# Optimization experiments

Hardware: AMD Instinct MI355X
Metric: run time of the kernel (lower is better)

The kernel has to match this reference:

```python
import jax, jax.numpy as jnp
import numpy as np

N_NODES = 50000
N_EDGES = 800000
D_IN = 512
D_OUT = 256


def setup_inputs() -> dict:
    key = jax.random.key(0)
    k1, k2, k3, k4, k5 = jax.random.split(key, 5)
    x = jax.random.normal(k1, (N_NODES, D_IN), dtype=jnp.float32)
    W = jax.random.normal(k2, (D_IN, D_OUT), dtype=jnp.float32) * (1.0 / np.sqrt(D_IN))
    edge_vals = jax.random.uniform(k3, (N_EDGES,), dtype=jnp.float32)
    edge_src = jax.random.randint(k4, (N_EDGES,), 0, N_NODES, dtype=jnp.int64)
    edge_dst = jax.random.randint(k5, (N_EDGES,), 0, N_NODES, dtype=jnp.int64)
    return {"x": x, "W": W, "edge_vals": edge_vals,
            "edge_src": edge_src, "edge_dst": edge_dst}


def reference(x, W, edge_vals, edge_src, edge_dst):
    # Dense feature transform: h = X W   [N, D_OUT]
    h = jnp.matmul(x, W)
    # Sparse adjacency matmul (A @ h) in COO form:
    # out[d] = sum_{e: dst[e]==d} vals[e] * h[src[e]]
    msgs = h[edge_src] * edge_vals[:, None]  # [E, D_OUT]
    agg = jax.ops.segment_sum(msgs, edge_dst, num_segments=N_NODES)
    # Activation ('relu')
    return jax.nn.relu(agg)
```

## Files before the change

kernel.cpp:

```cpp
#include <hip/hip_runtime.h>

typedef unsigned short u16;
typedef unsigned int   u32;
typedef __attribute__((ext_vector_type(8))) short bf16x8;
typedef __attribute__((ext_vector_type(4))) float f32x4;
typedef __attribute__((ext_vector_type(4))) unsigned short u16x4;

#define N_NODES 50000
#define N_EDGES 800000
#define D_IN    512
#define D_OUT   256
#define M_PAD   50048
#define NB_SCAN 196

__device__ __forceinline__ u16 f2bf(float f) {
  u32 u = __float_as_uint(f);
  return (u16)((u + 0x7FFFu + ((u >> 16) & 1u)) >> 16);
}
__device__ __forceinline__ u32 f2bf2(float lo, float hi) {
  return (u32)f2bf(lo) | ((u32)f2bf(hi) << 16);
}
__device__ __forceinline__ float bf2f(u16 h) {
  return __uint_as_float(((u32)h) << 16);
}

__device__ __forceinline__ void gload_lds16(const void* g, void* l) {
  __builtin_amdgcn_global_load_lds(
      (const __attribute__((address_space(1))) unsigned int*)g,
      (__attribute__((address_space(3))) unsigned int*)l, 16, 0, 0);
}

__global__ void k_init(int* __restrict__ counts, const float* __restrict__ W,
                       u16* __restrict__ wt) {
  int b = blockIdx.x;
  if (b < NB_SCAN) {
    int i = b * 256 + threadIdx.x;
    if (i < N_NODES) counts[i] = 0;
  } else {
    int g = (b - NB_SCAN) * 256 + threadIdx.x;
    int n = g & 255, k = g >> 8;
    wt[n * D_IN + k] = f2bf(W[k * D_OUT + n]);
  }
}

__global__ __launch_bounds__(512) void k_gemm_hist(
    const float* __restrict__ X, const u16* __restrict__ Bt,
    u16* __restrict__ C, int M,
    const int* __restrict__ edst, int* __restrict__ counts,
    int* __restrict__ rank, int E, int ngemm) {
  if ((int)blockIdx.x >= ngemm) {
    int e = ((int)blockIdx.x - ngemm) * 512 + threadIdx.x;
    if (e < E) rank[e] = atomicAdd(&counts[edst[e]], 1);
    return;
  }

  __shared__ u16 As[128 * 64];
  __shared__ u16 Bs[256 * 64];
  int tid  = threadIdx.x;
  int wave = tid >> 6, lane = tid & 63;
  int m0 = blockIdx.x * 128;
  int wr = wave >> 2, wc = wave & 3;
  int r = lane & 15, q = lane >> 4;

  int arow = tid >> 2, aq = tid & 3;
  int grow = m0 + arow;
  bool avalid = grow < M;
  const float* xrow = X + (size_t)grow * D_IN + aq * 16;
  u16* adst = As + arow * 64 + aq * 16;

  f32x4 acc[4][4];
#pragma unroll
  for (int i = 0; i < 4; ++i)
#pragma unroll
    for (int j = 0; j < 4; ++j) acc[i][j] = (f32x4){0.f, 0.f, 0.f, 0.f};

  for (int k0 = 0; k0 < D_IN; k0 += 64) {
#pragma unroll
    for (int j = 0; j < 4; ++j) {
      int c = tid + j * 512;
      int brow = c >> 3, bk = c & 7;
      gload_lds16(Bt + (size_t)brow * D_IN + k0 + bk * 8, Bs + c * 8);
    }
    uint4 w0 = {0u,0u,0u,0u}, w1 = {0u,0u,0u,0u};
    if (avalid) {
      float4 f0 = *(const float4*)(xrow + k0);
      float4 f1 = *(const float4*)(xrow + k0 + 4);
      float4 f2 = *(const float4*)(xrow + k0 + 8);
      float4 f3 = *(const float4*)(xrow + k0 + 12);
      w0.x = f2bf2(f0.x, f0.y);  w0.y = f2bf2(f0.z, f0.w);
      w0.z = f2bf2(f1.x, f1.y);  w0.w = f2bf2(f1.z, f1.w);
      w1.x = f2bf2(f2.x, f2.y);  w1.y = f2bf2(f2.z, f2.w);
      w1.z = f2bf2(f3.x, f3.y);  w1.w = f2bf2(f3.z, f3.w);
    }
    *(uint4*)(adst)     = w0;
    *(uint4*)(adst + 8) = w1;
    __syncthreads();
#pragma unroll
    for (int kk = 0; kk < 2; ++kk) {
      bf16x8 a[4], b[4];
#pragma unroll
      for (int i = 0; i < 4; ++i)
        a[i] = *(const bf16x8*)(As + (wr * 64 + i * 16 + r) * 64 + kk * 32 + q * 8);
#pragma unroll
      for (int j = 0; j < 4; ++j)
        b[j] = *(const bf16x8*)(Bs + (wc * 64 + j * 16 + r) * 64 + kk * 32 + q * 8);
#pragma unroll
      for (int i = 0; i < 4; ++i)
#pragma unroll
        for (int j = 0; j < 4; ++j)
          acc[i][j] = __builtin_amdgcn_mfma_f32_16x16x32_bf16(a[i], b[j], acc[i][j], 0, 0, 0);
    }
    __syncthreads();
  }

#pragma unroll
  for (int i = 0; i < 4; ++i)
#pragma unroll
    for (int j = 0; j < 4; ++j)
#pragma unroll
      for (int t2 = 0; t2 < 4; ++t2) {
        int row = m0 + wr * 64 + i * 16 + q * 4 + t2;
        int col = wc * 64 + j * 16 + r;
        if (row < M) C[(size_t)row * D_OUT + col] = f2bf(acc[i][j][t2]);
      }
}

__global__ void k_scan1(const int* __restrict__ counts, int* __restrict__ row_start,
                        int* __restrict__ btot, int n) {
  __shared__ int buf[256];
  int t = threadIdx.x;
  int i = blockIdx.x * 256 + t;
  int c = (i < n) ? counts[i] : 0;
  buf[t] = c;
  __syncthreads();
#pragma unroll
  for (int off = 1; off < 256; off <<= 1) {
    int v = (t >= off) ? buf[t - off] : 0;
    __syncthreads();
    buf[t] += v;
    __syncthreads();
  }
  if (i < n) row_start[i + 1] = buf[t];
  if (t == 255) btot[blockIdx.x] = buf[255];
}

__global__ void k_scan2(int* __restrict__ btot, int nb) {
  __shared__ int buf[256];
  int t = threadIdx.x;
  int c = (t < nb) ? btot[t] : 0;
  buf[t] = c;
  __syncthreads();
#pragma unroll
  for (int off = 1; off < 256; off <<= 1) {
    int v = (t >= off) ? buf[t - off] : 0;
    __syncthreads();
    buf[t] += v;
    __syncthreads();
  }
  if (t < nb) btot[t] = buf[t] - c;
}

__global__ void k_scan3(int* __restrict__ row_start, const int* __restrict__ btot, int n) {
  int i = blockIdx.x * blockDim.x + threadIdx.x;
  if (i < n) row_start[i + 1] += btot[i >> 8];
  if (i == 0) row_start[0] = 0;
}

__global__ void k_scatter(const int* __restrict__ esrc, const int* __restrict__ edst,
                          const float* __restrict__ ev, const int* __restrict__ row_start,
                          const int* __restrict__ rank,
                          int2* __restrict__ pack, int E) {
  int e = blockIdx.x * blockDim.x + threadIdx.x;
  if (e < E) {
    int pos = row_start[edst[e]] + rank[e];
    pack[pos] = make_int2(esrc[e], __float_as_int(ev[e]));
  }
}

__global__ __launch_bounds__(256) void k_agg(
    const u16* __restrict__ hb, const int* __restrict__ row_start,
    const int2* __restrict__ pack, float* __restrict__ out, int n_nodes) {
  int wave = threadIdx.x >> 6, lane = threadIdx.x & 63;
  int node = blockIdx.x * 4 + wave;
  if (node >= n_nodes) return;
  int s0 = row_start[node], s1 = row_start[node + 1];
  int cnt = s1 - s0;

  f32x4 a0 = {0.f,0.f,0.f,0.f}, a1 = {0.f,0.f,0.f,0.f};
  f32x4 a2 = {0.f,0.f,0.f,0.f}, a3 = {0.f,0.f,0.f,0.f};
  size_t lane8 = (size_t)lane * 8;

  for (int base = 0; base < cnt; base += 64) {
    int m = cnt - base; if (m > 64) m = 64;
    int   msrc = 0;
    float mval = 0.f;
    if (lane < m) {
      int2 p = pack[s0 + base + lane];
      msrc = p.x;
      mval = __uint_as_float((u32)p.y);
    }
    int k = 0;
    for (; k + 16 <= m; k += 16) {
      int   s[16];
      float v[16];
#pragma unroll
      for (int j = 0; j < 16; ++j) {
        s[j] = __shfl(msrc, k + j);
        v[j] = __shfl(mval, k + j);
      }
      u16x4 h[16];
#pragma unroll
      for (int j = 0; j < 16; ++j)
        h[j] = *(const u16x4*)((const char*)hb + (((size_t)(u32)s[j]) << 9) + lane8);
#pragma unroll
      for (int j = 0; j < 16; ++j) {
        f32x4* a = (j & 2) ? ((j & 1) ? &a3 : &a2) : ((j & 1) ? &a1 : &a0);
        (*a)[0] += v[j] * bf2f(h[j][0]);
        (*a)[1] += v[j] * bf2f(h[j][1]);
        (*a)[2] += v[j] * bf2f(h[j][2]);
        (*a)[3] += v[j] * bf2f(h[j][3]);
      }
    }
    for (; k + 4 <= m; k += 4) {
      int   s[4];
      float v[4];
#pragma unroll
      for (int j = 0; j < 4; ++j) {
        s[j] = __shfl(msrc, k + j);
        v[j] = __shfl(mval, k + j);
      }
      u16x4 h[4];
#pragma unroll
      for (int j = 0; j < 4; ++j)
        h[j] = *(const u16x4*)((const char*)hb + (((size_t)(u32)s[j]) << 9) + lane8);
#pragma unroll
      for (int j = 0; j < 4; ++j) {
        f32x4* a = (j & 1) ? &a1 : &a0;
        (*a)[0] += v[j] * bf2f(h[j][0]);
        (*a)[1] += v[j] * bf2f(h[j][1]);
        (*a)[2] += v[j] * bf2f(h[j][2]);
        (*a)[3] += v[j] * bf2f(h[j][3]);
      }
    }
    for (; k < m; ++k) {
      int   s = __shfl(msrc, k);
      float v = __shfl(mval, k);
      u16x4 h = *(const u16x4*)((const char*)hb + (((size_t)(u32)s) << 9) + lane8);
      a0[0] += v * bf2f(h[0]);
      a0[1] += v * bf2f(h[1]);
      a0[2] += v * bf2f(h[2]);
      a0[3] += v * bf2f(h[3]);
    }
  }
  float4 o;
  o.x = fmaxf(a0[0] + a1[0] + a2[0] + a3[0], 0.f);
  o.y = fmaxf(a0[1] + a1[1] + a2[1] + a3[1], 0.f);
  o.z = fmaxf(a0[2] + a1[2] + a2[2] + a3[2], 0.f);
  o.w = fmaxf(a0[3] + a1[3] + a2[3] + a3[3], 0.f);
  *(float4*)(out + (size_t)node * D_OUT + lane * 4) = o;
}

extern "C" void kernel_launch(void* const* d_in, const int* in_sizes, int n_in,
                              void* d_out, int out_size, void* d_ws, size_t ws_size,
                              hipStream_t stream) {
  const float* x    = (const float*)d_in[0];
  const float* W    = (const float*)d_in[1];
  const float* ev   = (const float*)d_in[2];
  const int*   esrc = (const int*)d_in[3];
  const int*   edst = (const int*)d_in[4];
  float* out = (float*)d_out;

  char* ws = (char*)d_ws;
  size_t off = 0;
  auto alloc = [&](size_t bytes) -> void* {
    off = (off + 255) & ~(size_t)255;
    void* p = ws + off;
    off += bytes;
    return p;
  };
  u16*   wt        = (u16*)  alloc((size_t)D_OUT * D_IN * 2);
  u16*   hb        = (u16*)  alloc((size_t)N_NODES * D_OUT * 2);
  int*   counts    = (int*)  alloc((size_t)N_NODES * 4);
  int*   row_start = (int*)  alloc((size_t)(N_NODES + 1) * 4);
  int*   rank      = (int*)  alloc((size_t)N_EDGES * 4);
  int*   btot      = (int*)  alloc(256 * 4);
  int2*  pack      = (int2*) alloc((size_t)N_EDGES * 8);

  int ngemm = M_PAD / 128;
  int nhist = (N_EDGES + 511) / 512;

  k_init<<<NB_SCAN + (D_IN * D_OUT) / 256, 256, 0, stream>>>(counts, W, wt);
  k_gemm_hist<<<ngemm + nhist, 512, 0, stream>>>(x, wt, hb, N_NODES,
                                                 edst, counts, rank, N_EDGES, ngemm);
  k_scan1<<<NB_SCAN, 256, 0, stream>>>(counts, row_start, btot, N_NODES);
  k_scan2<<<1, 256, 0, stream>>>(btot, NB_SCAN);
  k_scan3<<<NB_SCAN, 256, 0, stream>>>(row_start, btot, N_NODES);
  k_scatter<<<N_EDGES / 256, 256, 0, stream>>>(esrc, edst, ev, row_start, rank, pack, N_EDGES);
  k_agg<<<(N_NODES + 3) / 4, 256, 0, stream>>>(hb, row_start, pack, out, N_NODES);
}
```

Measured before the change: 139.0 us.

## Swizzle GEMM LDS tiles and gather two edges per wave with 16-byte loads

The GEMM stores and reads its A and B LDS tiles with an XOR swizzle on the 8-element k-chunk index. This is meant to remove LDS bank conflicts on the MFMA operand reads. The aggregation kernel now splits each wave into two half-waves, each handling a different edge and loading 16 bytes (8 bf16) per lane instead of 8, then combines the halves with a cross-half shuffle. This halves the number of gather instructions per edge and issues wider loads, at the cost of fewer independent accumulators and an extra reduction step.

```diff
diff --git a/kernel.cpp b/kernel.cpp
--- a/kernel.cpp
+++ b/kernel.cpp
@@ -4,7 +4,7 @@
 typedef unsigned int   u32;
 typedef __attribute__((ext_vector_type(8))) short bf16x8;
 typedef __attribute__((ext_vector_type(4))) float f32x4;
-typedef __attribute__((ext_vector_type(4))) unsigned short u16x4;
+typedef __attribute__((ext_vector_type(8))) unsigned short u16x8;
 
 #define N_NODES 50000
 #define N_EDGES 800000
@@ -66,7 +66,8 @@
   int grow = m0 + arow;
   bool avalid = grow < M;
   const float* xrow = X + (size_t)grow * D_IN + aq * 16;
-  u16* adst = As + arow * 64 + aq * 16;
+  u16* adst0 = As + arow * 64 + (((aq * 2)     ^ (arow & 7)) * 8);
+  u16* adst1 = As + arow * 64 + (((aq * 2 + 1) ^ (arow & 7)) * 8);
 
   f32x4 acc[4][4];
 #pragma unroll
@@ -78,7 +79,8 @@
 #pragma unroll
     for (int j = 0; j < 4; ++j) {
       int c = tid + j * 512;
-      int brow = c >> 3, bk = c & 7;
+      int brow = c >> 3, bslot = c & 7;
+      int bk = bslot ^ (brow & 7);
       gload_lds16(Bt + (size_t)brow * D_IN + k0 + bk * 8, Bs + c * 8);
     }
     uint4 w0 = {0u,0u,0u,0u}, w1 = {0u,0u,0u,0u};
@@ -92,18 +94,22 @@
       w1.x = f2bf2(f2.x, f2.y);  w1.y = f2bf2(f2.z, f2.w);
       w1.z = f2bf2(f3.x, f3.y);  w1.w = f2bf2(f3.z, f3.w);
     }
-    *(uint4*)(adst)     = w0;
-    *(uint4*)(adst + 8) = w1;
+    *(uint4*)(adst0) = w0;
+    *(uint4*)(adst1) = w1;
     __syncthreads();
 #pragma unroll
     for (int kk = 0; kk < 2; ++kk) {
       bf16x8 a[4], b[4];
 #pragma unroll
-      for (int i = 0; i < 4; ++i)
-        a[i] = *(const bf16x8*)(As + (wr * 64 + i * 16 + r) * 64 + kk * 32 + q * 8);
-#pragma unroll
-      for (int j = 0; j < 4; ++j)
-        b[j] = *(const bf16x8*)(Bs + (wc * 64 + j * 16 + r) * 64 + kk * 32 + q * 8);
+      for (int i = 0; i < 4; ++i) {
+        int ar = wr * 64 + i * 16 + r;
+        a[i] = *(const bf16x8*)(As + ar * 64 + (((kk * 4 + q) ^ (ar & 7)) * 8));
+      }
+#pragma unroll
+      for (int j = 0; j < 4; ++j) {
+        int br = wc * 64 + j * 16 + r;
+        b[j] = *(const bf16x8*)(Bs + br * 64 + (((kk * 4 + q) ^ (br & 7)) * 8));
+      }
 #pragma unroll
       for (int i = 0; i < 4; ++i)
 #pragma unroll
@@ -185,10 +191,12 @@
   if (node >= n_nodes) return;
   int s0 = row_start[node], s1 = row_start[node + 1];
   int cnt = s1 - s0;
-
-  f32x4 a0 = {0.f,0.f,0.f,0.f}, a1 = {0.f,0.f,0.f,0.f};
-  f32x4 a2 = {0.f,0.f,0.f,0.f}, a3 = {0.f,0.f,0.f,0.f};
-  size_t lane8 = (size_t)lane * 8;
+  int lane16 = lane & 31, half = lane >> 5;
+  size_t lanebyte = (size_t)lane16 * 16;
+
+  float acc[8];
+#pragma unroll
+  for (int c = 0; c < 8; ++c) acc[c] = 0.f;
 
   for (int base = 0; base < cnt; base += 64) {
     int m = cnt - base; if (m > 64) m = 64;
@@ -201,63 +209,44 @@
     }
     int k = 0;
     for (; k + 16 <= m; k += 16) {
-      int   s[16];
-      float v[16];
-#pragma unroll
-      for (int j = 0; j < 16; ++j) {
-        s[j] = __shfl(msrc, k + j);
-        v[j] = __shfl(mval, k + j);
-      }
-      u16x4 h[16];
-#pragma unroll
-      for (int j = 0; j < 16; ++j)
-        h[j] = *(const u16x4*)((const char*)hb + (((size_t)(u32)s[j]) << 9) + lane8);
-#pragma unroll
-      for (int j = 0; j < 16; ++j) {
-        f32x4* a = (j & 2) ? ((j & 1) ? &a3 : &a2) : ((j & 1) ? &a1 : &a0);
-        (*a)[0] += v[j] * bf2f(h[j][0]);
-        (*a)[1] += v[j] * bf2f(h[j][1]);
-        (*a)[2] += v[j] * bf2f(h[j][2]);
-        (*a)[3] += v[j] * bf2f(h[j][3]);
-      }
-    }
-    for (; k + 4 <= m; k += 4) {
-      int   s[4];
-      float v[4];
-#pragma unroll
-      for (int j = 0; j < 4; ++j) {
-        s[j] = __shfl(msrc, k + j);
-        v[j] = __shfl(mval, k + j);
-      }
-      u16x4 h[4];
-#pragma unroll
-      for (int j = 0; j < 4; ++j)
-        h[j] = *(const u16x4*)((const char*)hb + (((size_t)(u32)s[j]) << 9) + lane8);
-#pragma unroll
-      for (int j = 0; j < 4; ++j) {
-        f32x4* a = (j & 1) ? &a1 : &a0;
-        (*a)[0] += v[j] * bf2f(h[j][0]);
-        (*a)[1] += v[j] * bf2f(h[j][1]);
-        (*a)[2] += v[j] * bf2f(h[j][2]);
-        (*a)[3] += v[j] * bf2f(h[j][3]);
-      }
-    }
-    for (; k < m; ++k) {
-      int   s = __shfl(msrc, k);
-      float v = __shfl(mval, k);
-      u16x4 h = *(const u16x4*)((const char*)hb + (((size_t)(u32)s) << 9) + lane8);
-      a0[0] += v * bf2f(h[0]);
-      a0[1] += v * bf2f(h[1]);
-      a0[2] += v * bf2f(h[2]);
-      a0[3] += v * bf2f(h[3]);
-    }
-  }
+      int   s[8];
+      float v[8];
+#pragma unroll
+      for (int j = 0; j < 8; ++j) {
+        int e = k + 2 * j + half;
+        s[j] = __shfl(msrc, e);
+        v[j] = __shfl(mval, e);
+      }
+      u16x8 h[8];
+#pragma unroll
+      for (int j = 0; j < 8; ++j)
+        h[j] = *(const u16x8*)((const char*)hb + (((size_t)(u32)s[j]) << 9) + lanebyte);
+#pragma unroll
+      for (int j = 0; j < 8; ++j)
+#pragma unroll
+        for (int c = 0; c < 8; ++c)
+          acc[c] += v[j] * bf2f(h[j][c]);
+    }
+    for (; k < m; k += 2) {
+      int e = k + half;
+      int   sv = __shfl(msrc, e);
+      float vv = __shfl(mval, e);
+      u16x8 h = *(const u16x8*)((const char*)hb + (((size_t)(u32)sv) << 9) + lanebyte);
+#pragma unroll
+      for (int c = 0; c < 8; ++c)
+        acc[c] += vv * bf2f(h[c]);
+    }
+  }
+#pragma unroll
+  for (int c = 0; c < 8; ++c)
+    acc[c] += __shfl_xor(acc[c], 32);
+
   float4 o;
-  o.x = fmaxf(a0[0] + a1[0] + a2[0] + a3[0], 0.f);
-  o.y = fmaxf(a0[1] + a1[1] + a2[1] + a3[1], 0.f);
-  o.z = fmaxf(a0[2] + a1[2] + a2[2] + a3[2], 0.f);
-  o.w = fmaxf(a0[3] + a1[3] + a2[3] + a3[3], 0.f);
-  *(float4*)(out + (size_t)node * D_OUT + lane * 4) = o;
+  o.x = fmaxf(acc[half * 4 + 0], 0.f);
+  o.y = fmaxf(acc[half * 4 + 1], 0.f);
+  o.z = fmaxf(acc[half * 4 + 2], 0.f);
+  o.w = fmaxf(acc[half * 4 + 3], 0.f);
+  *(float4*)(out + (size_t)node * D_OUT + lane16 * 8 + half * 4) = o;
 }
 
 extern "C" void kernel_launch(void* const* d_in, const int* in_sizes, int n_in,
```

Result: no change. 137.6 us (-1.0%).
